# Optimization experiments

Measured on AMD Instinct MI355X. Metric: run time of the kernel, lower is better.

The kernel has to match this reference:

```python
import jax, jax.numpy as jnp
import numpy as np

R_MAX = 5.0
AVG_NEI = 16.0
NB = 8
L_OF_LM = np.repeat(np.arange(4), [1, 3, 5, 7])  # lm index -> l, 16 components for l_max=3


def real_sph(u):
    # real spherical harmonics up to l=3, component normalization; u: [E,3] unit vectors
    x, y, z = u[:, 0], u[:, 1], u[:, 2]
    x2, y2, z2 = x * x, y * y, z * z
    return jnp.stack([
        jnp.ones_like(x),
        1.7320508 * x, 1.7320508 * y, 1.7320508 * z,
        3.8729833 * x * y, 3.8729833 * y * z,
        1.1180340 * (3.0 * z2 - 1.0),
        3.8729833 * x * z, 1.9364917 * (x2 - y2),
        2.0916500 * y * (3.0 * x2 - y2), 10.246951 * x * y * z,
        1.6201852 * y * (5.0 * z2 - 1.0), 1.3228757 * z * (5.0 * z2 - 3.0),
        1.6201852 * x * (5.0 * z2 - 1.0), 5.1234753 * z * (x2 - y2),
        2.0916500 * x * (x2 - 3.0 * y2),
    ], axis=-1)


def radial_embed(r):
    # Bessel basis * polynomial (p=5) envelope, as in MACE RadialEmbeddingBlock
    n = jnp.arange(1, NB + 1, dtype=r.dtype)
    bess = jnp.sqrt(2.0 / R_MAX) * jnp.sin(n * jnp.pi * r[:, None] / R_MAX) / (r[:, None] + 1e-8)
    p = 5.0
    t = jnp.clip(r / R_MAX, 0.0, 1.0)
    env = 1.0 - 0.5 * (p + 1) * (p + 2) * t**p + p * (p + 2) * t**(p + 1) - 0.5 * p * (p + 1) * t**(p + 2)
    return bess * env[:, None]


def interaction(feats, Y, R, senders, receivers, Wu, Wd, num_nodes):
    # feats: [N,C,Din] (Din = sum of (2l+1) over input l-blocks); Y: [E,16]; R: [E,C,12] radial path weights
    n_lin = Wu.shape[0]
    up = jnp.concatenate([
        jnp.einsum('ncm,cd->ndm', feats[:, :, l * l:(l + 1) * (l + 1)], Wu[l])
        for l in range(n_lin)], axis=-1)
    hs = up[senders]  # gather sender features [E,C,Din]
    R0, R1, R2 = R[..., 0:4], R[..., 4:8], R[..., 8:12]
    # CG path (0, l_sh) -> l_sh : scalar feature times Y_l
    msg = R0[:, :, L_OF_LM] * hs[:, :, 0:1] * Y[:, None, :]  # [E,C,16]
    for l in range(1, n_lin):
        sl = slice(l * l, (l + 1) * (l + 1))
        # CG path (l, 0) -> l
        msg = msg.at[:, :, sl].add(R1[:, :, l:l + 1] * hs[:, :, sl] * Y[:, None, 0:1])
        # CG path (l, l) -> 0 : invariant dot product
        msg = msg.at[:, :, 0].add(R2[:, :, l] * jnp.sum(hs[:, :, sl] * Y[:, None, sl], axis=-1))
    agg = jnp.zeros((num_nodes, msg.shape[1], msg.shape[2]), msg.dtype).at[receivers].add(msg) / AVG_NEI
    return jnp.einsum('ncm,mcd->ndm', agg, Wd[L_OF_LM])  # per-l linear down


def setup_inputs() -> dict:
    key = jax.random.key(0)
    ks = jax.random.split(key, 18)
    N, E, C, S = 10000, 160000, 64, 10
    f32 = jnp.float32
    rn = lambda k, shape, scale: jax.random.normal(k, shape, f32) * scale
    return {
        'edge_vectors': rn(ks[0], (E, 3), 1.5),
        'node_embed': rn(ks[1], (S, C), 0.3),
        'rw1': rn(ks[2], (2, NB, 64), 1.0 / np.sqrt(NB)),
        'rw2': rn(ks[3], (2, 64, C * 12), 1.0 / np.sqrt(64)),
        'lu0': rn(ks[4], (1, C, C), 1.0 / np.sqrt(C)),
        'lu1': rn(ks[5], (2, C, C), 1.0 / np.sqrt(C)),
        'ld': rn(ks[6], (2, 4, C, C), 1.0 / np.sqrt(C)),
        'sel_w': rn(ks[7], (S, 4, C, C), 1.0 / np.sqrt(C)),
        'prod_w0': rn(ks[8], (S, C, C), 1.0 / np.sqrt(C)),
        'prod_w1': rn(ks[9], (S, C, C), 1.0 / np.sqrt(C)),
        'res_w': rn(ks[10], (S, C, C), 1.0 / np.sqrt(C)),
        'read0': rn(ks[11], (C, 1), 1.0 / np.sqrt(C)),
        'mlp_w1': rn(ks[12], (C, 32), 1.0 / np.sqrt(C)),
        'mlp_w2': rn(ks[13], (32, 1), 1.0 / np.sqrt(32)),
        'node_species': jax.random.randint(ks[14], (N,), 0, S),
        'senders': jax.random.randint(ks[15], (E,), 0, N),
        'receivers': jax.random.randint(ks[16], (E,), 0, N),
    }


def reference(edge_vectors, node_embed, rw1, rw2, lu0, lu1, ld, sel_w, prod_w0,
              prod_w1, res_w, read0, mlp_w1, mlp_w2, node_species, senders, receivers):
    N = node_species.shape[0]
    C = node_embed.shape[1]
    r = jnp.linalg.norm(edge_vectors, axis=-1)
    u = edge_vectors / (r[:, None] + 1e-8)
    Y = real_sph(u)                      # [E,16]
    rb = radial_embed(r)                 # [E,8]
    R_all = [(jax.nn.silu(rb @ rw1[i]) @ rw2[i]).reshape(-1, C, 12) for i in range(2)]
    # ---- layer 0 (selector_tp, not last) ----
    f = node_embed[node_species][:, :, None]               # [N,C,1] scalar embed
    f = interaction(f, Y, R_all[0], senders, receivers, lu0, ld[0], N)  # [N,C,16]
    blocks = []
    for l in range(4):  # species-dependent selector TP (per-l channel mixing)
        sl = slice(l * l, (l + 1) * (l + 1))
        blocks.append(jnp.einsum('ncm,ncd->ndm', f[:, :, sl], sel_w[node_species, l]))
    f = jnp.concatenate(blocks, axis=-1)
    # product basis (correlation 3 polynomial in invariant channel), target C x (0e+1o)
    s = f[:, :, 0]
    f1 = jnp.einsum('ncm,ncd->ndm', f[:, :, :4] * (1.0 + s + s * s)[:, :, None], prod_w0[node_species])
    out0 = f1[:, :, 0] @ read0           # linear readout head  [N,1]
    # ---- layer 1 (last, residual) ----
    res = jnp.einsum('nc,ncd->nd', f1[:, :, 0], res_w[node_species])
    g = interaction(f1, Y, R_all[1], senders, receivers, lu1, ld[1], N)  # [N,C,16]
    inv = g[:, :, 0] + jnp.sum(g[:, :, 1:] ** 2, axis=-1)  # invariants from all l blocks
    f2 = jnp.einsum('nc,ncd->nd', inv + inv * inv, prod_w1[node_species]) + res
    out1 = jax.nn.silu(f2 @ mlp_w1) @ mlp_w2  # nonlinear readout  [N,1]
    # stack heads (axis=2) then layers (axis=1): [N, num_interactions, num_heads, 1]
    return jnp.stack([out0, out1], axis=1)[:, :, None, :]
```

## Files before the change

### kernel.cpp

```cpp
#include <hip/hip_runtime.h>
#include <math.h>


#define LANES 64

typedef _Float16 half8 __attribute__((ext_vector_type(8)));
typedef _Float16 half4v __attribute__((ext_vector_type(4)));
typedef float f32x4 __attribute__((ext_vector_type(4)));

__device__ __forceinline__ float silu_f(float x) { return x / (1.0f + expf(-x)); }

__device__ __forceinline__ float reduce64(float v) {
#pragma unroll
  for (int off = 32; off > 0; off >>= 1) v += __shfl_xor(v, off, LANES);
  return v;
}

__device__ __forceinline__ int l_of_m(int m) {
  return (m == 0) ? 0 : ((m < 4) ? 1 : ((m < 9) ? 2 : 3));
}

__device__ __forceinline__ void compute_Y(float x, float y, float z, float* Y) {
  float x2 = x * x, y2 = y * y, z2 = z * z;
  Y[0] = 1.0f;
  Y[1] = 1.7320508f * x;
  Y[2] = 1.7320508f * y;
  Y[3] = 1.7320508f * z;
  Y[4] = 3.8729833f * x * y;
  Y[5] = 3.8729833f * y * z;
  Y[6] = 1.118034f * (3.0f * z2 - 1.0f);
  Y[7] = 3.8729833f * x * z;
  Y[8] = 1.9364917f * (x2 - y2);
  Y[9] = 2.09165f * y * (3.0f * x2 - y2);
  Y[10] = 10.246951f * x * y * z;
  Y[11] = 1.6201852f * y * (5.0f * z2 - 1.0f);
  Y[12] = 1.3228757f * z * (5.0f * z2 - 3.0f);
  Y[13] = 1.6201852f * x * (5.0f * z2 - 1.0f);
  Y[14] = 5.1234753f * z * (x2 - y2);
  Y[15] = 2.09165f * x * (x2 - 3.0f * y2);
}

__device__ __forceinline__ void compute_rb(float r, float inv_r, float* rb) {
  float t = fminf(r * 0.2f, 1.0f);
  float t2 = t * t;
  float t5 = t2 * t2 * t;
  float env = 1.0f + t5 * (-21.0f + t * (35.0f - 15.0f * t));
  float th = 0.62831853f * r;
  float s1 = sinf(th), c1 = cosf(th);
  float c2 = 2.0f * c1;
  float sprev = 0.0f, scur = s1;
  float coef = 0.63245553f * inv_r * env;
#pragma unroll
  for (int k = 0; k < 8; k++) {
    rb[k] = coef * scur;
    float snxt = c2 * scur - sprev;
    sprev = scur;
    scur = snxt;
  }
}

__global__ __launch_bounds__(256) void k_hist(const int* __restrict__ receivers,
                                              int* __restrict__ cnt, int E) {
  int e = blockIdx.x * 256 + threadIdx.x;
  if (e < E) atomicAdd(&cnt[receivers[e]], 1);
}

__global__ __launch_bounds__(256) void k_scan(const int* __restrict__ deg,
                                              int* __restrict__ row_start,
                                              int* __restrict__ cursor, int N) {
  __shared__ int part[256];
  int t = threadIdx.x;
  int K = (N + 255) / 256;
  int lo = t * K, hi = min(lo + K, N);
  int s = 0;
  for (int i = lo; i < hi; i++) s += deg[i];
  part[t] = s;
  __syncthreads();
  for (int d = 1; d < 256; d <<= 1) {
    int v = (t >= d) ? part[t - d] : 0;
    __syncthreads();
    part[t] += v;
    __syncthreads();
  }
  int run = (t == 0) ? 0 : part[t - 1];
  for (int i = lo; i < hi; i++) {
    int di = deg[i];
    row_start[i] = run;
    cursor[i] = run;
    run += di;
  }
  if (t == 255) row_start[N] = part[255];
}

__global__ __launch_bounds__(256) void k_scatter(const int* __restrict__ receivers,
                                                 const int* __restrict__ senders,
                                                 int* __restrict__ cursor,
                                                 int* __restrict__ perm,
                                                 int* __restrict__ rsort,
                                                 int* __restrict__ ssort, int E) {
  int e = blockIdx.x * 256 + threadIdx.x;
  if (e < E) {
    int r = receivers[e];
    int pos = atomicAdd(&cursor[r], 1);
    perm[pos] = e;
    rsort[pos] = r;
    ssort[pos] = senders[e];
  }
}

__global__ __launch_bounds__(256) void k_pack(const float* __restrict__ rw2,
                                              const float* __restrict__ ldw,
                                              _Float16* __restrict__ b1t,
                                              _Float16* __restrict__ b2t,
                                              _Float16* __restrict__ ld1t) {
  int idx = blockIdx.x * 256 + threadIdx.x;
  if (idx < 8192) {
    int n = idx >> 6, k = idx & 63;
    int c = n >> 1, j = n & 1;
    b1t[idx] = (_Float16)rw2[k * 768 + c * 12 + j];
  } else if (idx < 32768) {
    int i2 = idx - 8192;
    int n = i2 >> 6, k = i2 & 63;
    int c = n / 6, j = n - c * 6;
    int col = (j < 4) ? j : ((j == 4) ? 5 : 9);
    b2t[i2] = (_Float16)rw2[49152 + k * 768 + c * 12 + col];
  } else if (idx < 49152) {
    int i3 = idx - 32768;
    int l = i3 >> 12;
    int rem = i3 & 4095;
    int dd = rem >> 6, cc = rem & 63;
    ld1t[i3] = (_Float16)ldw[16384 + (l << 12) + (cc << 6) + dd];
  }
}

__global__ __launch_bounds__(256) void k_up0(const float* __restrict__ embed,
                                             const float* __restrict__ lu0,
                                             const int* __restrict__ species,
                                             float* __restrict__ up0, int N) {
  int wave = threadIdx.x >> 6, lane = threadIdx.x & 63;
  int n = (blockIdx.x << 2) + wave;
  if (n >= N) return;
  int sp = species[n];
  const float* er = embed + sp * 64;
  float acc = 0.0f;
#pragma unroll 8
  for (int c = 0; c < 64; c++) acc += er[c] * lu0[c * 64 + lane];
  up0[(size_t)n * 64 + lane] = acc;
}

__global__ __launch_bounds__(256) void k_geom(const float* __restrict__ ev,
                                              const float* __restrict__ rw1,
                                              const int* __restrict__ perm,
                                              _Float16* __restrict__ hid0,
                                              _Float16* __restrict__ hid1,
                                              float* __restrict__ Ysort,
                                              int* __restrict__ rsort,
                                              int* __restrict__ ssort,
                                              int E, int EPAD) {
  int wave = threadIdx.x >> 6, lane = threadIdx.x & 63;
  int j = blockIdx.x * 4 + wave;
  if (j >= EPAD) return;
  if (j >= E) {
    hid0[(size_t)j * 64 + lane] = (_Float16)0.0f;
    hid1[(size_t)j * 64 + lane] = (_Float16)0.0f;
    if (lane == 0) { rsort[j] = -1; ssort[j] = 0; }
    if (lane < 16) Ysort[(size_t)j * 16 + lane] = 0.0f;
    return;
  }
  int e = perm[j];
  float vx = ev[e * 3 + 0], vy = ev[e * 3 + 1], vz = ev[e * 3 + 2];
  float r = sqrtf(vx * vx + vy * vy + vz * vz);
  float inv_r = 1.0f / (r + 1e-8f);
  float Y[16];
  compute_Y(vx * inv_r, vy * inv_r, vz * inv_r, Y);
  float rb[8];
  compute_rb(r, inv_r, rb);

  float h0 = 0.0f, h1 = 0.0f;
#pragma unroll
  for (int k = 0; k < 8; k++) {
    h0 += rb[k] * rw1[k * 64 + lane];
    h1 += rb[k] * rw1[512 + k * 64 + lane];
  }
  hid0[(size_t)j * 64 + lane] = (_Float16)silu_f(h0);
  hid1[(size_t)j * 64 + lane] = (_Float16)silu_f(h1);

  float yv = Y[0];
#pragma unroll
  for (int m = 1; m < 16; m++) yv = (lane == m) ? Y[m] : yv;
  if (lane < 16) Ysort[(size_t)j * 16 + lane] = yv;
}

__global__ __launch_bounds__(256) void k_fagg1(const _Float16* __restrict__ hid,
                                               const _Float16* __restrict__ bt,
                                               const float* __restrict__ Ysort,
                                               const float* __restrict__ up0,
                                               const int* __restrict__ ssort,
                                               const int* __restrict__ rsort,
                                               float* __restrict__ agg1c, int E) {
  __shared__ _Float16 __attribute__((aligned(16))) lds[4][16 * 128];
  int wave = threadIdx.x >> 6, lane = threadIdx.x & 63;
  int q = lane >> 4, mr = lane & 15;
  _Float16* L = lds[wave];
  int j0 = __builtin_amdgcn_readfirstlane((blockIdx.x * 4 + wave) * 16);

  int rs[16], ss[16];
#pragma unroll
  for (int t = 0; t < 16; t++) {
    rs[t] = rsort[j0 + t];
    ss[t] = ssort[j0 + t];
  }
  float hsv[16];
#pragma unroll
  for (int t = 0; t < 16; t++) hsv[t] = up0[((size_t)ss[t] << 6) + lane];

  const half8* Ap = (const half8*)(hid + (size_t)(j0 + mr) * 64 + q * 8);
  half8 a0 = Ap[0];
  half8 a1 = Ap[4];
  const _Float16* bp = bt + (size_t)mr * 64 + q * 8;
#pragma unroll
  for (int T = 0; T < 8; T++) {
    half8 b0 = *(const half8*)(bp + T * 1024);
    half8 b1 = *(const half8*)(bp + T * 1024 + 32);
    f32x4 acc = {0.f, 0.f, 0.f, 0.f};
    acc = __builtin_amdgcn_mfma_f32_16x16x32_f16(a0, b0, acc, 0, 0, 0);
    acc = __builtin_amdgcn_mfma_f32_16x16x32_f16(a1, b1, acc, 0, 0, 0);
#pragma unroll
    for (int r = 0; r < 4; r++)
      L[(q * 4 + r) * 128 + T * 16 + mr] = (_Float16)acc[r];
  }

  float accm[4] = {0.f, 0.f, 0.f, 0.f};
  int cur_r = (j0 < E) ? rs[0] : -1;

#pragma unroll
  for (int t = 0; t < 16; t++) {
    int j = j0 + t;
    bool ok = (j < E);
    int rr = ok ? rs[t] : -2;
    if (rr != cur_r) {
      if (cur_r >= 0) {
        float* base = agg1c + ((size_t)cur_r << 8) + lane;
#pragma unroll
        for (int m = 0; m < 4; m++) atomicAdd(base + (m << 6), accm[m]);
      }
#pragma unroll
      for (int m = 0; m < 4; m++) accm[m] = 0.0f;
      cur_r = rr;
    }
    if (ok) {
      float hs0 = hsv[t];
      const _Float16* Rr = L + t * 128 + lane * 2;
      float p0 = (float)Rr[0] * hs0;
      float p1 = (float)Rr[1] * hs0;
      float4 Ya = *(const float4*)(Ysort + (size_t)j * 16);
      accm[0] += p0;
      accm[1] += p1 * Ya.y;
      accm[2] += p1 * Ya.z;
      accm[3] += p1 * Ya.w;
    }
  }
  if (cur_r >= 0) {
    float* base = agg1c + ((size_t)cur_r << 8) + lane;
#pragma unroll
    for (int m = 0; m < 4; m++) atomicAdd(base + (m << 6), accm[m]);
  }
}

__global__ __launch_bounds__(256, 3) void k_fagg2(const _Float16* __restrict__ hid,
                                                  const _Float16* __restrict__ bt,
                                                  const float* __restrict__ Ysort,
                                                  const _Float16* __restrict__ up1,
                                                  const int* __restrict__ ssort,
                                                  const int* __restrict__ rsort,
                                                  float* __restrict__ agg, int E) {
  __shared__ _Float16 __attribute__((aligned(16))) lds[4][16 * 384];
  int wave = threadIdx.x >> 6, lane = threadIdx.x & 63;
  int q = lane >> 4, mr = lane & 15;
  _Float16* L = lds[wave];
  int j0 = __builtin_amdgcn_readfirstlane((blockIdx.x * 4 + wave) * 16);

  int rs[16], ss[16];
#pragma unroll
  for (int t = 0; t < 16; t++) {
    rs[t] = rsort[j0 + t];
    ss[t] = ssort[j0 + t];
  }
  half4v hA[8];
#pragma unroll
  for (int t = 0; t < 8; t++)
    hA[t] = *(const half4v*)(up1 + ((size_t)ss[t] << 8) + lane * 4);

  const half8* Ap = (const half8*)(hid + (size_t)(j0 + mr) * 64 + q * 8);
  half8 a0 = Ap[0];
  half8 a1 = Ap[4];
  const _Float16* bp = bt + (size_t)mr * 64 + q * 8;
#pragma unroll
  for (int T = 0; T < 24; T++) {
    half8 b0 = *(const half8*)(bp + T * 1024);
    half8 b1 = *(const half8*)(bp + T * 1024 + 32);
    f32x4 acc = {0.f, 0.f, 0.f, 0.f};
    acc = __builtin_amdgcn_mfma_f32_16x16x32_f16(a0, b0, acc, 0, 0, 0);
    acc = __builtin_amdgcn_mfma_f32_16x16x32_f16(a1, b1, acc, 0, 0, 0);
#pragma unroll
    for (int r = 0; r < 4; r++)
      L[(q * 4 + r) * 384 + T * 16 + mr] = (_Float16)acc[r];
  }

  half4v hB[8];
#pragma unroll
  for (int t = 0; t < 8; t++)
    hB[t] = *(const half4v*)(up1 + ((size_t)ss[8 + t] << 8) + lane * 4);

  float accm[16];
#pragma unroll
  for (int m = 0; m < 16; m++) accm[m] = 0.0f;
  int cur_r = (j0 < E) ? rs[0] : -1;

#pragma unroll
  for (int t = 0; t < 16; t++) {
    int j = j0 + t;
    bool ok = (j < E);
    int rr = ok ? rs[t] : -2;
    if (rr != cur_r) {
      if (cur_r >= 0) {
        float* base = agg + ((size_t)cur_r << 10) + lane;
#pragma unroll
        for (int m = 0; m < 16; m++) atomicAdd(base + (m << 6), accm[m]);
      }
#pragma unroll
      for (int m = 0; m < 16; m++) accm[m] = 0.0f;
      cur_r = rr;
    }
    if (ok) {
      half4v hs = (t < 8) ? hA[t & 7] : hB[t & 7];
      float hs0 = (float)hs.x, hs1 = (float)hs.y;
      float hs2 = (float)hs.z, hs3 = (float)hs.w;
      const _Float16* Rr = L + t * 384 + lane * 6;
      float R0 = (float)Rr[0], R1v = (float)Rr[1];
      float R2v = (float)Rr[2], R3v = (float)Rr[3];
      float c5 = (float)Rr[4], c9 = (float)Rr[5];
      float q0 = R0 * hs0, q1 = R1v * hs0, q2 = R2v * hs0, q3 = R3v * hs0;
      const float* Yj = Ysort + (size_t)j * 16;
      float4 Ya = *(const float4*)(Yj);
      float4 Yb = *(const float4*)(Yj + 4);
      float4 Yc = *(const float4*)(Yj + 8);
      float4 Yd = *(const float4*)(Yj + 12);
      accm[0] += q0 + c9 * (hs1 * Ya.y + hs2 * Ya.z + hs3 * Ya.w);
      accm[1] += q1 * Ya.y + c5 * hs1;
      accm[2] += q1 * Ya.z + c5 * hs2;
      accm[3] += q1 * Ya.w + c5 * hs3;
      accm[4] += q2 * Yb.x;
      accm[5] += q2 * Yb.y;
      accm[6] += q2 * Yb.z;
      accm[7] += q2 * Yb.w;
      accm[8] += q2 * Yc.x;
      accm[9] += q3 * Yc.y;
      accm[10] += q3 * Yc.z;
      accm[11] += q3 * Yc.w;
      accm[12] += q3 * Yd.x;
      accm[13] += q3 * Yd.y;
      accm[14] += q3 * Yd.z;
      accm[15] += q3 * Yd.w;
    }
  }
  if (cur_r >= 0) {
    float* base = agg + ((size_t)cur_r << 10) + lane;
#pragma unroll
    for (int m = 0; m < 16; m++) atomicAdd(base + (m << 6), accm[m]);
  }
}

__global__ __launch_bounds__(64) void k_node1(const float* __restrict__ agg1c,
                                              const float* __restrict__ ld0,
                                              const float* __restrict__ sel_w,
                                              const float* __restrict__ pw0,
                                              const float* __restrict__ res_w,
                                              const float* __restrict__ lu1,
                                              const float* __restrict__ read0,
                                              const int* __restrict__ species,
                                              float* __restrict__ out,
                                              float* __restrict__ res,
                                              _Float16* __restrict__ up1, int N) {
  int n = blockIdx.x, d = threadIdx.x;
  int sp = species[n];
  __shared__ float sA[256], sB[256];

  const float* ag = agg1c + ((size_t)n << 8);
#pragma unroll
  for (int m = 0; m < 4; m++) sA[m * 64 + d] = ag[(m << 6) + d] * 0.0625f;
  __syncthreads();

  float fr[4] = {0.f, 0.f, 0.f, 0.f};
  {
    const float* W0 = ld0 + d;
    const float* W1 = ld0 + 4096 + d;
#pragma unroll 8
    for (int c = 0; c < 64; c++) {
      float w0 = W0[c * 64], w1 = W1[c * 64];
      fr[0] += sA[c] * w0;
      fr[1] += sA[64 + c] * w1;
      fr[2] += sA[128 + c] * w1;
      fr[3] += sA[192 + c] * w1;
    }
  }
#pragma unroll
  for (int m = 0; m < 4; m++) sB[m * 64 + d] = fr[m];
  __syncthreads();

  float f2r[4] = {0.f, 0.f, 0.f, 0.f};
  {
    const float* W0 = sel_w + ((size_t)(sp * 4) << 12) + d;
    const float* W1 = sel_w + ((size_t)(sp * 4 + 1) << 12) + d;
#pragma unroll 8
    for (int c = 0; c < 64; c++) {
      float w0 = W0[c * 64], w1 = W1[c * 64];
      f2r[0] += sB[c] * w0;
      f2r[1] += sB[64 + c] * w1;
      f2r[2] += sB[128 + c] * w1;
      f2r[3] += sB[192 + c] * w1;
    }
  }
  float s0 = f2r[0];
  float tt = 1.0f + s0 + s0 * s0;
#pragma unroll
  for (int m = 0; m < 4; m++) sA[m * 64 + d] = f2r[m] * tt;
  __syncthreads();

  float f1r[4] = {0.f, 0.f, 0.f, 0.f};
  {
    const float* W = pw0 + ((size_t)sp << 12) + d;
#pragma unroll 8
    for (int c = 0; c < 64; c++) {
      float w = W[c * 64];
#pragma unroll
      for (int m = 0; m < 4; m++) f1r[m] += sA[m * 64 + c] * w;
    }
  }
#pragma unroll
  for (int m = 0; m < 4; m++) sB[m * 64 + d] = f1r[m];
  __syncthreads();

  float v = reduce64(f1r[0] * read0[d]);
  if (d == 0) out[2 * n] = v;

  float u0;
  {
    const float* Wr = res_w + ((size_t)sp << 12) + d;
    const float* Wu = lu1 + d;
    float a = 0.0f, b = 0.0f;
#pragma unroll 8
    for (int c = 0; c < 64; c++) {
      float fv = sB[c];
      a += fv * Wr[c * 64];
      b += fv * Wu[c * 64];
    }
    res[((size_t)n << 6) + d] = a;
    u0 = b;
  }
  {
    const float* Wu = lu1 + 4096 + d;
    float a1 = 0.f, a2 = 0.f, a3 = 0.f;
#pragma unroll 8
    for (int c = 0; c < 64; c++) {
      float w = Wu[c * 64];
      a1 += sB[64 + c] * w;
      a2 += sB[128 + c] * w;
      a3 += sB[192 + c] * w;
    }
    half4v uu;
    uu.x = (_Float16)u0;
    uu.y = (_Float16)a1;
    uu.z = (_Float16)a2;
    uu.w = (_Float16)a3;
    *(half4v*)(up1 + ((size_t)n << 8) + d * 4) = uu;
  }
}

__global__ __launch_bounds__(256) void k_node2(const float* __restrict__ agg1,
                                               const _Float16* __restrict__ ld1t,
                                               const float* __restrict__ pw1,
                                               const float* __restrict__ res,
                                               const float* __restrict__ mlp_w1,
                                               const float* __restrict__ mlp_w2,
                                               const int* __restrict__ species,
                                               float* __restrict__ out, int N) {
  __shared__ float sq[16 * 65];
  __shared__ float sf[16 * 65];
  int tid = threadIdx.x;
  int wave = tid >> 6, lane = tid & 63;
  int q = lane >> 4, mr = lane & 15;
  int nb = blockIdx.x * 16;

  int arow = min(nb + mr, N - 1);
  const float* Arow = agg1 + ((size_t)arow << 10);

  float inv[4] = {0.f, 0.f, 0.f, 0.f};
#pragma unroll
  for (int m = 0; m < 16; m++) {
    int l = l_of_m(m);
    const float* ap = Arow + (m << 6) + q * 8;
    half8 a0, a1;
#pragma unroll
    for (int i = 0; i < 8; i++) {
      a0[i] = (_Float16)(ap[i] * 0.0625f);
      a1[i] = (_Float16)(ap[32 + i] * 0.0625f);
    }
    const _Float16* bp = ld1t + (l << 12) + ((wave * 16 + mr) << 6) + q * 8;
    half8 b0 = *(const half8*)(bp);
    half8 b1 = *(const half8*)(bp + 32);
    f32x4 acc = {0.f, 0.f, 0.f, 0.f};
    acc = __builtin_amdgcn_mfma_f32_16x16x32_f16(a0, b0, acc, 0, 0, 0);
    acc = __builtin_amdgcn_mfma_f32_16x16x32_f16(a1, b1, acc, 0, 0, 0);
    if (m == 0) {
#pragma unroll
      for (int r = 0; r < 4; r++) inv[r] += acc[r];
    } else {
#pragma unroll
      for (int r = 0; r < 4; r++) inv[r] += acc[r] * acc[r];
    }
  }
#pragma unroll
  for (int r = 0; r < 4; r++) {
    float iv = inv[r];
    sq[(q * 4 + r) * 65 + wave * 16 + mr] = iv + iv * iv;
  }
  __syncthreads();

  int d = lane;
#pragma unroll
  for (int g = 0; g < 4; g++) {
    int nl = wave + 4 * g;
    int n = nb + nl;
    int nc = min(n, N - 1);
    int sp = species[nc];
    float a = res[((size_t)nc << 6) + d];
    const float* W = pw1 + ((size_t)sp << 12) + d;
#pragma unroll 8
    for (int c = 0; c < 64; c++) a += sq[nl * 65 + c] * W[c * 64];
    sf[nl * 65 + d] = a;
  }
  __syncthreads();

#pragma unroll
  for (int p = 0; p < 2; p++) {
    int nl = wave * 2 + (lane >> 5) + p * 8;
    int n = nb + nl;
    int h = lane & 31;
    float hh = 0.f;
#pragma unroll 8
    for (int c = 0; c < 64; c++) hh += sf[nl * 65 + c] * mlp_w1[c * 32 + h];
    float val = silu_f(hh) * mlp_w2[h];
#pragma unroll
    for (int off = 16; off > 0; off >>= 1) val += __shfl_xor(val, off, 64);
    if (h == 0 && n < N) out[2 * n + 1] = val;
  }
}

extern "C" void kernel_launch(void* const* d_in, const int* in_sizes, int n_in,
                              void* d_out, int out_size, void* d_ws, size_t ws_size,
                              hipStream_t stream) {
  const float* ev      = (const float*)d_in[0];
  const float* embed   = (const float*)d_in[1];
  const float* rw1     = (const float*)d_in[2];
  const float* rw2     = (const float*)d_in[3];
  const float* lu0     = (const float*)d_in[4];
  const float* lu1     = (const float*)d_in[5];
  const float* ld      = (const float*)d_in[6];
  const float* sel_w   = (const float*)d_in[7];
  const float* pw0     = (const float*)d_in[8];
  const float* pw1     = (const float*)d_in[9];
  const float* res_w   = (const float*)d_in[10];
  const float* read0   = (const float*)d_in[11];
  const float* mlp_w1  = (const float*)d_in[12];
  const float* mlp_w2  = (const float*)d_in[13];
  const int* species   = (const int*)d_in[14];
  const int* senders   = (const int*)d_in[15];
  const int* receivers = (const int*)d_in[16];
  float* out = (float*)d_out;

  int N = in_sizes[14];
  int E = in_sizes[15];
  int EPAD = ((E + 63) / 64) * 64;

  float* ws = (float*)d_ws;
  size_t o = 0;
  float* agg   = ws + o;  o += (size_t)N * 1024;
  float* agg1c = ws + o;  o += (size_t)N * 256;
  float* up0   = ws + o;  o += (size_t)N * 64;
  _Float16* up1 = (_Float16*)(ws + o); o += (size_t)N * 128;
  float* resb  = ws + o;  o += (size_t)N * 64;
  _Float16* b1t  = (_Float16*)(ws + o); o += 4096;
  _Float16* b2t  = (_Float16*)(ws + o); o += 12288;
  _Float16* ld1t = (_Float16*)(ws + o); o += 8192;
  _Float16* hid0 = (_Float16*)(ws + o); o += (size_t)EPAD * 32;
  _Float16* hid1 = (_Float16*)(ws + o); o += (size_t)EPAD * 32;
  float* Ysort = ws + o;  o += (size_t)EPAD * 16;
  int* row_start = (int*)(ws + o); o += (size_t)N + 1;
  int* cursor    = (int*)(ws + o); o += (size_t)N;
  int* perm      = (int*)(ws + o); o += (size_t)E;
  int* rsort     = (int*)(ws + o); o += (size_t)EPAD;
  int* ssort     = (int*)(ws + o); o += (size_t)EPAD;

  hipMemsetAsync(agg, 0, (size_t)N * 1280 * sizeof(float), stream);
  hipMemsetAsync(cursor, 0, (size_t)N * sizeof(int), stream);

  k_hist<<<(E + 255) / 256, 256, 0, stream>>>(receivers, cursor, E);
  k_scan<<<1, 256, 0, stream>>>(cursor, row_start, cursor, N);
  k_scatter<<<(E + 255) / 256, 256, 0, stream>>>(receivers, senders, cursor,
                                                 perm, rsort, ssort, E);

  k_pack<<<192, 256, 0, stream>>>(rw2, ld, b1t, b2t, ld1t);
  k_up0<<<(N + 3) / 4, 256, 0, stream>>>(embed, lu0, species, up0, N);
  k_geom<<<EPAD / 4, 256, 0, stream>>>(ev, rw1, perm, hid0, hid1, Ysort,
                                       rsort, ssort, E, EPAD);

  int fblocks = EPAD / 64;
  k_fagg1<<<fblocks, 256, 0, stream>>>(hid0, b1t, Ysort, up0, ssort, rsort,
                                       agg1c, E);
  k_node1<<<N, 64, 0, stream>>>(agg1c, ld, sel_w, pw0, res_w, lu1, read0,
                                species, out, resb, up1, N);
  k_fagg2<<<fblocks, 256, 0, stream>>>(hid1, b2t, Ysort, up1, ssort, rsort,
                                       agg, E);
  k_node2<<<(N + 15) / 16, 256, 0, stream>>>(agg, ld1t, pw1, resb, mlp_w1,
                                             mlp_w2, species, out, N);
}
```

Before: 408.6 us.

## Assign one wave per receiver node in edge aggregation, dropping atomics and memset

```diff
diff --git a/kernel.cpp b/kernel.cpp
--- a/kernel.cpp
+++ b/kernel.cpp
@@ -96,14 +96,12 @@
                                                  const int* __restrict__ senders,
                                                  int* __restrict__ cursor,
                                                  int* __restrict__ perm,
-                                                 int* __restrict__ rsort,
                                                  int* __restrict__ ssort, int E) {
   int e = blockIdx.x * 256 + threadIdx.x;
   if (e < E) {
     int r = receivers[e];
     int pos = atomicAdd(&cursor[r], 1);
     perm[pos] = e;
-    rsort[pos] = r;
     ssort[pos] = senders[e];
   }
 }
@@ -154,7 +152,6 @@
                                               _Float16* __restrict__ hid0,
                                               _Float16* __restrict__ hid1,
                                               float* __restrict__ Ysort,
-                                              int* __restrict__ rsort,
                                               int* __restrict__ ssort,
                                               int E, int EPAD) {
   int wave = threadIdx.x >> 6, lane = threadIdx.x & 63;
@@ -163,7 +160,7 @@
   if (j >= E) {
     hid0[(size_t)j * 64 + lane] = (_Float16)0.0f;
     hid1[(size_t)j * 64 + lane] = (_Float16)0.0f;
-    if (lane == 0) { rsort[j] = -1; ssort[j] = 0; }
+    if (lane == 0) ssort[j] = 0;
     if (lane < 16) Ysort[(size_t)j * 16 + lane] = 0.0f;
     return;
   }
@@ -196,59 +193,48 @@
                                                const float* __restrict__ Ysort,
                                                const float* __restrict__ up0,
                                                const int* __restrict__ ssort,
-                                               const int* __restrict__ rsort,
-                                               float* __restrict__ agg1c, int E) {
+                                               const int* __restrict__ row_start,
+                                               float* __restrict__ agg1c, int N) {
   __shared__ _Float16 __attribute__((aligned(16))) lds[4][16 * 128];
   int wave = threadIdx.x >> 6, lane = threadIdx.x & 63;
   int q = lane >> 4, mr = lane & 15;
   _Float16* L = lds[wave];
-  int j0 = __builtin_amdgcn_readfirstlane((blockIdx.x * 4 + wave) * 16);
-
-  int rs[16], ss[16];
-#pragma unroll
-  for (int t = 0; t < 16; t++) {
-    rs[t] = rsort[j0 + t];
-    ss[t] = ssort[j0 + t];
-  }
-  float hsv[16];
-#pragma unroll
-  for (int t = 0; t < 16; t++) hsv[t] = up0[((size_t)ss[t] << 6) + lane];
-
-  const half8* Ap = (const half8*)(hid + (size_t)(j0 + mr) * 64 + q * 8);
-  half8 a0 = Ap[0];
-  half8 a1 = Ap[4];
-  const _Float16* bp = bt + (size_t)mr * 64 + q * 8;
-#pragma unroll
-  for (int T = 0; T < 8; T++) {
-    half8 b0 = *(const half8*)(bp + T * 1024);
-    half8 b1 = *(const half8*)(bp + T * 1024 + 32);
-    f32x4 acc = {0.f, 0.f, 0.f, 0.f};
-    acc = __builtin_amdgcn_mfma_f32_16x16x32_f16(a0, b0, acc, 0, 0, 0);
-    acc = __builtin_amdgcn_mfma_f32_16x16x32_f16(a1, b1, acc, 0, 0, 0);
-#pragma unroll
-    for (int r = 0; r < 4; r++)
-      L[(q * 4 + r) * 128 + T * 16 + mr] = (_Float16)acc[r];
-  }
+  int n = blockIdx.x * 4 + wave;
+  if (n >= N) return;
+  int rs = __builtin_amdgcn_readfirstlane(row_start[n]);
+  int re = __builtin_amdgcn_readfirstlane(row_start[n + 1]);
+  int ntile = (re - rs + 15) >> 4;
 
   float accm[4] = {0.f, 0.f, 0.f, 0.f};
-  int cur_r = (j0 < E) ? rs[0] : -1;
-
-#pragma unroll
-  for (int t = 0; t < 16; t++) {
-    int j = j0 + t;
-    bool ok = (j < E);
-    int rr = ok ? rs[t] : -2;
-    if (rr != cur_r) {
-      if (cur_r >= 0) {
-        float* base = agg1c + ((size_t)cur_r << 8) + lane;
-#pragma unroll
-        for (int m = 0; m < 4; m++) atomicAdd(base + (m << 6), accm[m]);
-      }
-#pragma unroll
-      for (int m = 0; m < 4; m++) accm[m] = 0.0f;
-      cur_r = rr;
-    }
-    if (ok) {
+
+  for (int k = 0; k < ntile; k++) {
+    int j0 = rs + k * 16;
+    int ss[16];
+#pragma unroll
+    for (int t = 0; t < 16; t++) ss[t] = ssort[j0 + t];
+    float hsv[16];
+#pragma unroll
+    for (int t = 0; t < 16; t++) hsv[t] = up0[((size_t)ss[t] << 6) + lane];
+
+    const half8* Ap = (const half8*)(hid + (size_t)(j0 + mr) * 64 + q * 8);
+    half8 a0 = Ap[0];
+    half8 a1 = Ap[4];
+    const _Float16* bp = bt + (size_t)mr * 64 + q * 8;
+#pragma unroll
+    for (int T = 0; T < 8; T++) {
+      half8 b0 = *(const half8*)(bp + T * 1024);
+      half8 b1 = *(const half8*)(bp + T * 1024 + 32);
+      f32x4 acc = {0.f, 0.f, 0.f, 0.f};
+      acc = __builtin_amdgcn_mfma_f32_16x16x32_f16(a0, b0, acc, 0, 0, 0);
+      acc = __builtin_amdgcn_mfma_f32_16x16x32_f16(a1, b1, acc, 0, 0, 0);
+#pragma unroll
+      for (int r = 0; r < 4; r++)
+        L[(q * 4 + r) * 128 + T * 16 + mr] = (_Float16)acc[r];
+    }
+
+    int lim = min(re - j0, 16);
+    for (int t = 0; t < lim; t++) {
+      int j = j0 + t;
       float hs0 = hsv[t];
       const _Float16* Rr = L + t * 128 + lane * 2;
       float p0 = (float)Rr[0] * hs0;
@@ -260,11 +246,10 @@
       accm[3] += p1 * Ya.w;
     }
   }
-  if (cur_r >= 0) {
-    float* base = agg1c + ((size_t)cur_r << 8) + lane;
-#pragma unroll
-    for (int m = 0; m < 4; m++) atomicAdd(base + (m << 6), accm[m]);
-  }
+
+  float* base = agg1c + ((size_t)n << 8) + lane;
+#pragma unroll
+  for (int m = 0; m < 4; m++) base[m << 6] = accm[m];
 }
 
 __global__ __launch_bounds__(256, 3) void k_fagg2(const _Float16* __restrict__ hid,
@@ -272,68 +257,52 @@
                                                   const float* __restrict__ Ysort,
                                                   const _Float16* __restrict__ up1,
                                                   const int* __restrict__ ssort,
-                                                  const int* __restrict__ rsort,
-                                                  float* __restrict__ agg, int E) {
+                                                  const int* __restrict__ row_start,
+                                                  float* __restrict__ agg, int N) {
   __shared__ _Float16 __attribute__((aligned(16))) lds[4][16 * 384];
   int wave = threadIdx.x >> 6, lane = threadIdx.x & 63;
   int q = lane >> 4, mr = lane & 15;
   _Float16* L = lds[wave];
-  int j0 = __builtin_amdgcn_readfirstlane((blockIdx.x * 4 + wave) * 16);
-
-  int rs[16], ss[16];
-#pragma unroll
-  for (int t = 0; t < 16; t++) {
-    rs[t] = rsort[j0 + t];
-    ss[t] = ssort[j0 + t];
-  }
-  half4v hA[8];
-#pragma unroll
-  for (int t = 0; t < 8; t++)
-    hA[t] = *(const half4v*)(up1 + ((size_t)ss[t] << 8) + lane * 4);
-
-  const half8* Ap = (const half8*)(hid + (size_t)(j0 + mr) * 64 + q * 8);
-  half8 a0 = Ap[0];
-  half8 a1 = Ap[4];
-  const _Float16* bp = bt + (size_t)mr * 64 + q * 8;
-#pragma unroll
-  for (int T = 0; T < 24; T++) {
-    half8 b0 = *(const half8*)(bp + T * 1024);
-    half8 b1 = *(const half8*)(bp + T * 1024 + 32);
-    f32x4 acc = {0.f, 0.f, 0.f, 0.f};
-    acc = __builtin_amdgcn_mfma_f32_16x16x32_f16(a0, b0, acc, 0, 0, 0);
-    acc = __builtin_amdgcn_mfma_f32_16x16x32_f16(a1, b1, acc, 0, 0, 0);
-#pragma unroll
-    for (int r = 0; r < 4; r++)
-      L[(q * 4 + r) * 384 + T * 16 + mr] = (_Float16)acc[r];
-  }
-
-  half4v hB[8];
-#pragma unroll
-  for (int t = 0; t < 8; t++)
-    hB[t] = *(const half4v*)(up1 + ((size_t)ss[8 + t] << 8) + lane * 4);
+  int n = blockIdx.x * 4 + wave;
+  if (n >= N) return;
+  int rs = __builtin_amdgcn_readfirstlane(row_start[n]);
+  int re = __builtin_amdgcn_readfirstlane(row_start[n + 1]);
+  int ntile = (re - rs + 15) >> 4;
 
   float accm[16];
 #pragma unroll
   for (int m = 0; m < 16; m++) accm[m] = 0.0f;
-  int cur_r = (j0 < E) ? rs[0] : -1;
-
-#pragma unroll
-  for (int t = 0; t < 16; t++) {
-    int j = j0 + t;
-    bool ok = (j < E);
-    int rr = ok ? rs[t] : -2;
-    if (rr != cur_r) {
-      if (cur_r >= 0) {
-        float* base = agg + ((size_t)cur_r << 10) + lane;
-#pragma unroll
-        for (int m = 0; m < 16; m++) atomicAdd(base + (m << 6), accm[m]);
-      }
-#pragma unroll
-      for (int m = 0; m < 16; m++) accm[m] = 0.0f;
-      cur_r = rr;
-    }
-    if (ok) {
-      half4v hs = (t < 8) ? hA[t & 7] : hB[t & 7];
+
+  for (int k = 0; k < ntile; k++) {
+    int j0 = rs + k * 16;
+    int ss[16];
+#pragma unroll
+    for (int t = 0; t < 16; t++) ss[t] = ssort[j0 + t];
+    half4v hv[16];
+#pragma unroll
+    for (int t = 0; t < 16; t++)
+      hv[t] = *(const half4v*)(up1 + ((size_t)ss[t] << 8) + lane * 4);
+
+    const half8* Ap = (const half8*)(hid + (size_t)(j0 + mr) * 64 + q * 8);
+    half8 a0 = Ap[0];
+    half8 a1 = Ap[4];
+    const _Float16* bp = bt + (size_t)mr * 64 + q * 8;
+#pragma unroll
+    for (int T = 0; T < 24; T++) {
+      half8 b0 = *(const half8*)(bp + T * 1024);
+      half8 b1 = *(const half8*)(bp + T * 1024 + 32);
+      f32x4 acc = {0.f, 0.f, 0.f, 0.f};
+      acc = __builtin_amdgcn_mfma_f32_16x16x32_f16(a0, b0, acc, 0, 0, 0);
+      acc = __builtin_amdgcn_mfma_f32_16x16x32_f16(a1, b1, acc, 0, 0, 0);
+#pragma unroll
+      for (int r = 0; r < 4; r++)
+        L[(q * 4 + r) * 384 + T * 16 + mr] = (_Float16)acc[r];
+    }
+
+    int lim = min(re - j0, 16);
+    for (int t = 0; t < lim; t++) {
+      int j = j0 + t;
+      half4v hs = hv[t];
       float hs0 = (float)hs.x, hs1 = (float)hs.y;
       float hs2 = (float)hs.z, hs3 = (float)hs.w;
       const _Float16* Rr = L + t * 384 + lane * 6;
@@ -364,11 +333,10 @@
       accm[15] += q3 * Yd.w;
     }
   }
-  if (cur_r >= 0) {
-    float* base = agg + ((size_t)cur_r << 10) + lane;
-#pragma unroll
-    for (int m = 0; m < 16; m++) atomicAdd(base + (m << 6), accm[m]);
-  }
+
+  float* base = agg + ((size_t)n << 10) + lane;
+#pragma unroll
+  for (int m = 0; m < 16; m++) base[m << 6] = accm[m];
 }
 
 __global__ __launch_bounds__(64) void k_node1(const float* __restrict__ agg1c,
@@ -581,7 +549,7 @@
 
   int N = in_sizes[14];
   int E = in_sizes[15];
-  int EPAD = ((E + 63) / 64) * 64;
+  int EPAD = ((E + 63 + 16) / 64) * 64;
 
   float* ws = (float*)d_ws;
   size_t o = 0;
@@ -599,29 +567,27 @@
   int* row_start = (int*)(ws + o); o += (size_t)N + 1;
   int* cursor    = (int*)(ws + o); o += (size_t)N;
   int* perm      = (int*)(ws + o); o += (size_t)E;
-  int* rsort     = (int*)(ws + o); o += (size_t)EPAD;
   int* ssort     = (int*)(ws + o); o += (size_t)EPAD;
 
-  hipMemsetAsync(agg, 0, (size_t)N * 1280 * sizeof(float), stream);
   hipMemsetAsync(cursor, 0, (size_t)N * sizeof(int), stream);
 
   k_hist<<<(E + 255) / 256, 256, 0, stream>>>(receivers, cursor, E);
   k_scan<<<1, 256, 0, stream>>>(cursor, row_start, cursor, N);
   k_scatter<<<(E + 255) / 256, 256, 0, stream>>>(receivers, senders, cursor,
-                                                 perm, rsort, ssort, E);
+                                                 perm, ssort, E);
 
   k_pack<<<192, 256, 0, stream>>>(rw2, ld, b1t, b2t, ld1t);
   k_up0<<<(N + 3) / 4, 256, 0, stream>>>(embed, lu0, species, up0, N);
   k_geom<<<EPAD / 4, 256, 0, stream>>>(ev, rw1, perm, hid0, hid1, Ysort,
-                                       rsort, ssort, E, EPAD);
-
-  int fblocks = EPAD / 64;
-  k_fagg1<<<fblocks, 256, 0, stream>>>(hid0, b1t, Ysort, up0, ssort, rsort,
-                                       agg1c, E);
+                                       ssort, E, EPAD);
+
+  int nblocks = (N + 3) / 4;
+  k_fagg1<<<nblocks, 256, 0, stream>>>(hid0, b1t, Ysort, up0, ssort, row_start,
+                                       agg1c, N);
   k_node1<<<N, 64, 0, stream>>>(agg1c, ld, sel_w, pw0, res_w, lu1, read0,
                                 species, out, resb, up1, N);
-  k_fagg2<<<fblocks, 256, 0, stream>>>(hid1, b2t, Ysort, up1, ssort, rsort,
-                                       agg, E);
+  k_fagg2<<<nblocks, 256, 0, stream>>>(hid1, b2t, Ysort, up1, ssort, row_start,
+                                       agg, N);
   k_node2<<<(N + 15) / 16, 256, 0, stream>>>(agg, ld1t, pw1, resb, mlp_w1,
                                              mlp_w2, species, out, N);
 }
```

Result: slower. 747.5 us (+83.0%).
